# Optimization experiments

Measured on AMD Instinct MI355X. Metric: run time of the kernel, lower is better.

## Reference

```python
import jax, jax.numpy as jnp
import numpy as np

TQ, T, D = 2048, 16384, 256
H, KD, VD, DOUT = 8, 32, 32, 256


def setup_inputs() -> dict:
    key = jax.random.key(0)
    ks = jax.random.split(key, 8)
    w_scale = 1.0 / np.sqrt(D)
    return {
        "query": jax.random.normal(ks[0], (TQ, D), dtype=jnp.float32),
        "key": jax.random.normal(ks[1], (T, D), dtype=jnp.float32),
        "value": jax.random.normal(ks[2], (T, D), dtype=jnp.float32),
        "wq": jax.random.normal(ks[3], (D, H * KD), dtype=jnp.float32) * w_scale,
        "bq": jnp.zeros((H * KD,), dtype=jnp.float32),
        "wk": jax.random.normal(ks[4], (D, H * KD), dtype=jnp.float32) * w_scale,
        "bk": jnp.zeros((H * KD,), dtype=jnp.float32),
        "wv": jax.random.normal(ks[5], (D, H * VD), dtype=jnp.float32) * w_scale,
        "bv": jnp.zeros((H * VD,), dtype=jnp.float32),
        "wo": jax.random.normal(ks[6], (H * VD, DOUT), dtype=jnp.float32) * (1.0 / np.sqrt(H * VD)),
        "bo": jnp.zeros((DOUT,), dtype=jnp.float32),
    }


def reference(query, key, value, wq, bq, wk, bk, wv, bv, wo, bo):
    # Linear projections to heads: [Tq,H,KD], [T,H,KD], [T,H,VD]
    qh = (query @ wq + bq).reshape(TQ, H, KD)
    kh = (key @ wk + bk).reshape(T, H, KD)
    vh = (value @ wv + bv).reshape(T, H, VD)
    # Chunked online-softmax attention == exact softmax attention.
    # Query scaled by 1/sqrt(head_dim) as in the memory-efficient impl.
    scale = np.float32(1.0 / np.sqrt(KD))
    logits = jnp.einsum("qhd,khd->hqk", qh * scale, kh)  # [H,Tq,T]
    weights = jax.nn.softmax(logits, axis=-1)
    attn = jnp.einsum("hqk,khd->qhd", weights, vh).reshape(TQ, H * VD)
    return attn @ wo + bo  # [Tq, DOUT]
```

## Files before the change

### kernel.cpp

```cpp
#include <hip/hip_runtime.h>
#include <stdint.h>


typedef float f32x4 __attribute__((ext_vector_type(4)));
typedef __bf16 bf16x8 __attribute__((ext_vector_type(8)));

extern "C" __device__ float __ocml_native_exp2_f32(float);

__device__ __forceinline__ unsigned short f2bf(float f) {
  unsigned int u = __builtin_bit_cast(unsigned int, f);
  u += 0x7FFFu + ((u >> 16) & 1u);
  return (unsigned short)(u >> 16);
}
__device__ __forceinline__ float bf2f(unsigned u) {
  return __builtin_bit_cast(float, u << 16);
}
__device__ __forceinline__ f32x4 mfma16(bf16x8 a, bf16x8 b, f32x4 c) {
  return __builtin_amdgcn_mfma_f32_16x16x32_bf16(a, b, c, 0, 0, 0);
}
__device__ __forceinline__ float ex2(float x) {
#if __has_builtin(__builtin_amdgcn_exp2f)
  return __builtin_amdgcn_exp2f(x);
#else
  return __ocml_native_exp2_f32(x);
#endif
}
__device__ __forceinline__ unsigned pk2(float a, float b) {
  unsigned short ua = __builtin_bit_cast(unsigned short, (__bf16)a);
  unsigned short ub = __builtin_bit_cast(unsigned short, (__bf16)b);
  return (unsigned)ua | ((unsigned)ub << 16);
}
__device__ __forceinline__ uint2 pack4(f32x4 a) {
  uint2 r;
  r.x = (unsigned)f2bf(a[0]) | ((unsigned)f2bf(a[1]) << 16);
  r.y = (unsigned)f2bf(a[2]) | ((unsigned)f2bf(a[3]) << 16);
  return r;
}

#define QSCALE 0.25503483f

__global__ __launch_bounds__(256) void convert_w_kernel(
    const float* __restrict__ wq, const float* __restrict__ wk,
    const float* __restrict__ wv, const float* __restrict__ wo,
    unsigned short* __restrict__ tq, unsigned short* __restrict__ tk,
    unsigned short* __restrict__ tv, unsigned short* __restrict__ to)
{
  const int mat = blockIdx.x >> 6, k0 = (blockIdx.x & 63) * 4, n = threadIdx.x;
  const float* src; unsigned short* dst;
  if (mat == 0) { src = wq; dst = tq; }
  else if (mat == 1) { src = wk; dst = tk; }
  else if (mat == 2) { src = wv; dst = tv; }
  else { src = wo; dst = to; }
  unsigned e0 = f2bf(src[(size_t)(k0 + 0) * 256 + n]);
  unsigned e1 = f2bf(src[(size_t)(k0 + 1) * 256 + n]);
  unsigned e2 = f2bf(src[(size_t)(k0 + 2) * 256 + n]);
  unsigned e3 = f2bf(src[(size_t)(k0 + 3) * 256 + n]);
  uint2 pk = { e0 | (e1 << 16), e2 | (e3 << 16) };
  *(uint2*)&dst[(size_t)n * 256 + k0] = pk;
}

__global__ __launch_bounds__(512) void proj4_kernel(
    const float* __restrict__ Xq, const float* __restrict__ Xk,
    const float* __restrict__ Xv,
    const unsigned short* __restrict__ Wtq, const unsigned short* __restrict__ Wtk,
    const unsigned short* __restrict__ Wtv,
    const float* __restrict__ Bq, const float* __restrict__ Bk,
    const float* __restrict__ Bv,
    unsigned short* __restrict__ Oq, unsigned short* __restrict__ Ok,
    unsigned short* __restrict__ Ov)
{
  const int mat = blockIdx.y;
  const float* X; const unsigned short* Wt; const float* Bp; unsigned short* Op;
  int N; float scale; int vmode;
  if (mat == 0) {
    if (blockIdx.x >= 32) return;
    X = Xq; Wt = Wtq; Bp = Bq; Op = Oq; N = 2048; scale = QSCALE; vmode = 0;
  } else if (mat == 1) {
    X = Xk; Wt = Wtk; Bp = Bk; Op = Ok; N = 16384; scale = 1.f; vmode = 0;
  } else {
    X = Xv; Wt = Wtv; Bp = Bv; Op = Ov; N = 16384; scale = 1.f; vmode = 1;
  }
  const int tid = threadIdx.x;
  const int w = tid >> 6, lane = tid & 63, g = lane >> 4, c = lane & 15;
  const int m0 = blockIdx.x * 64;

  __shared__ __align__(16) unsigned short Xs[64 * 40];
  __shared__ __align__(16) unsigned short Ws[256 * 40];

  const f32x4 zero4 = {0.f, 0.f, 0.f, 0.f};
  f32x4 acc[4][2];
  #pragma unroll
  for (int i = 0; i < 4; ++i) { acc[i][0] = zero4; acc[i][1] = zero4; }

  const int xrow = tid >> 3, xseg = (tid & 7) * 4;
  const int wrow = tid >> 1, wseg = (tid & 1) * 16;

  for (int k0 = 0; k0 < 256; k0 += 32) {
    if (k0) __syncthreads();
    {
      float4 x = *(const float4*)&X[(size_t)(m0 + xrow) * 256 + k0 + xseg];
      uint2 px = { pk2(x.x, x.y), pk2(x.z, x.w) };
      *(uint2*)&Xs[xrow * 40 + xseg] = px;
    }
    {
      const unsigned short* wp = Wt + (size_t)wrow * 256 + k0 + wseg;
      int4 w0 = *(const int4*)wp;
      int4 w1 = *(const int4*)(wp + 8);
      *(int4*)&Ws[wrow * 40 + wseg] = w0;
      *(int4*)&Ws[wrow * 40 + wseg + 8] = w1;
    }
    __syncthreads();

    bf16x8 a[4], b[2];
    #pragma unroll
    for (int rt = 0; rt < 4; ++rt)
      a[rt] = *(const bf16x8*)&Xs[(16 * rt + c) * 40 + 8 * g];
    #pragma unroll
    for (int ct = 0; ct < 2; ++ct)
      b[ct] = *(const bf16x8*)&Ws[(32 * w + 16 * ct + c) * 40 + 8 * g];
    #pragma unroll
    for (int rt = 0; rt < 4; ++rt)
      #pragma unroll
      for (int ct = 0; ct < 2; ++ct)
        acc[rt][ct] = mfma16(a[rt], b[ct], acc[rt][ct]);
  }

  #pragma unroll
  for (int ct = 0; ct < 2; ++ct) {
    const int col = 32 * w + 16 * ct + c;
    const float bv = Bp[col];
    const int hh = col >> 5, d = col & 31;
    #pragma unroll
    for (int rt = 0; rt < 4; ++rt)
      #pragma unroll
      for (int r = 0; r < 4; ++r) {
        const int row = m0 + 16 * rt + 4 * g + r;
        const unsigned short v = f2bf((acc[rt][ct][r] + bv) * scale);
        if (vmode) {
          const int pr = (row & ~31) | (((row >> 3) & 1) << 4) |
                         (((row >> 2) & 1) << 3) | (((row >> 4) & 1) << 2) |
                         (row & 3);
          Op[((size_t)hh * 32 + d) * (size_t)N + pr] = v;
        } else {
          Op[((size_t)hh * N + row) * 32 + d] = v;
        }
      }
  }
}

__global__ __launch_bounds__(256) void attn6_kernel(
    const unsigned short* __restrict__ qh, const unsigned short* __restrict__ kh,
    const unsigned short* __restrict__ vth,
    unsigned short* __restrict__ part_o, float* __restrict__ part_l)
{
  const int f = blockIdx.x + 16 * (blockIdx.y + 8 * blockIdx.z);
  const int v = (f & 7) * 128 + (f >> 3);
  const int qb = v & 15, h = (v >> 4) & 7, sp = v >> 7;

  const int tid = threadIdx.x;
  const int w = tid >> 6, lane = tid & 63, g = lane >> 4, c = lane & 15;
  const int q0 = qb * 128 + w * 32;

  __shared__ __align__(16) unsigned short K0a[64 * 40], K0b[64 * 40];
  __shared__ __align__(16) unsigned short K1a[64 * 40], K1b[64 * 40];
  __shared__ __align__(16) unsigned short V0a[32 * 72], V0b[32 * 72];
  __shared__ __align__(16) unsigned short V1a[32 * 72], V1b[32 * 72];

  const bf16x8 qf0 = *(const bf16x8*)&qh[((size_t)h * 2048 + q0 + c) * 32 + 8 * g];
  const bf16x8 qf1 = *(const bf16x8*)&qh[((size_t)h * 2048 + q0 + 16 + c) * 32 + 8 * g];

  bf16x8 ones;
  #pragma unroll
  for (int j = 0; j < 8; ++j) ones[j] = (__bf16)1.0f;

  const f32x4 zero4 = {0.f, 0.f, 0.f, 0.f};
  f32x4 acc00 = zero4, acc01 = zero4, acc10 = zero4, acc11 = zero4;
  f32x4 accL0 = zero4, accL1 = zero4;

  const int skey = tid >> 2, sseg = (tid & 3) * 8;
  const int kwoff = skey * 40 + sseg;
  const int vrow = tid >> 3, vseg = (tid & 7) * 8;
  const int vwoff = vrow * 72 + vseg;

  const unsigned short* kp = kh + (size_t)h * 524288 +
                             ((size_t)(sp * 2048) + skey) * 32 + sseg;
  const unsigned short* vp = vth + ((size_t)h * 32 + vrow) * 16384 +
                             sp * 2048 + vseg;

  auto compute = [&](const unsigned short* Kb, const unsigned short* Vb) {
    bf16x8 kf0 = *(const bf16x8*)&Kb[(c) * 40 + 8 * g];
    bf16x8 kf1 = *(const bf16x8*)&Kb[(16 + c) * 40 + 8 * g];
    bf16x8 kf2 = *(const bf16x8*)&Kb[(32 + c) * 40 + 8 * g];
    bf16x8 kf3 = *(const bf16x8*)&Kb[(48 + c) * 40 + 8 * g];
    f32x4 s0 = mfma16(kf0, qf0, zero4);
    f32x4 s1 = mfma16(kf1, qf0, zero4);
    f32x4 s2 = mfma16(kf2, qf0, zero4);
    f32x4 s3 = mfma16(kf3, qf0, zero4);
    f32x4 t0 = mfma16(kf0, qf1, zero4);
    f32x4 t1 = mfma16(kf1, qf1, zero4);
    f32x4 t2 = mfma16(kf2, qf1, zero4);
    f32x4 t3 = mfma16(kf3, qf1, zero4);

    union { unsigned u[4]; bf16x8 v; } pa00, pa01, pa10, pa11;
    pa00.u[0] = pk2(ex2(s0[0]), ex2(s0[1]));
    pa00.u[1] = pk2(ex2(s0[2]), ex2(s0[3]));
    pa00.u[2] = pk2(ex2(s1[0]), ex2(s1[1]));
    pa00.u[3] = pk2(ex2(s1[2]), ex2(s1[3]));
    pa01.u[0] = pk2(ex2(s2[0]), ex2(s2[1]));
    pa01.u[1] = pk2(ex2(s2[2]), ex2(s2[3]));
    pa01.u[2] = pk2(ex2(s3[0]), ex2(s3[1]));
    pa01.u[3] = pk2(ex2(s3[2]), ex2(s3[3]));
    pa10.u[0] = pk2(ex2(t0[0]), ex2(t0[1]));
    pa10.u[1] = pk2(ex2(t0[2]), ex2(t0[3]));
    pa10.u[2] = pk2(ex2(t1[0]), ex2(t1[1]));
    pa10.u[3] = pk2(ex2(t1[2]), ex2(t1[3]));
    pa11.u[0] = pk2(ex2(t2[0]), ex2(t2[1]));
    pa11.u[1] = pk2(ex2(t2[2]), ex2(t2[3]));
    pa11.u[2] = pk2(ex2(t3[0]), ex2(t3[1]));
    pa11.u[3] = pk2(ex2(t3[2]), ex2(t3[3]));

    bf16x8 v00 = *(const bf16x8*)&Vb[c * 72 + 8 * g];
    bf16x8 v01 = *(const bf16x8*)&Vb[c * 72 + 32 + 8 * g];
    bf16x8 v10 = *(const bf16x8*)&Vb[(16 + c) * 72 + 8 * g];
    bf16x8 v11 = *(const bf16x8*)&Vb[(16 + c) * 72 + 32 + 8 * g];
    __builtin_amdgcn_s_setprio(1);
    acc00 = mfma16(v00, pa00.v, acc00);
    acc01 = mfma16(v10, pa00.v, acc01);
    accL0 = mfma16(ones, pa00.v, accL0);
    acc00 = mfma16(v01, pa01.v, acc00);
    acc01 = mfma16(v11, pa01.v, acc01);
    accL0 = mfma16(ones, pa01.v, accL0);
    acc10 = mfma16(v00, pa10.v, acc10);
    acc11 = mfma16(v10, pa10.v, acc11);
    accL1 = mfma16(ones, pa10.v, accL1);
    acc10 = mfma16(v01, pa11.v, acc10);
    acc11 = mfma16(v11, pa11.v, acc11);
    accL1 = mfma16(ones, pa11.v, accL1);
    __builtin_amdgcn_s_setprio(0);
  };

  {
    int4 ka = *(const int4*)kp;
    int4 va = *(const int4*)vp;
    int4 kb = *(const int4*)(kp + 2048);
    int4 vb = *(const int4*)(vp + 64);
    *(int4*)&K0a[kwoff] = ka;
    *(int4*)&V0a[vwoff] = va;
    *(int4*)&K0b[kwoff] = kb;
    *(int4*)&V0b[vwoff] = vb;
  }
  int4 kr0 = *(const int4*)(kp + 2 * 2048);
  int4 vr0 = *(const int4*)(vp + 2 * 64);
  int4 kr1 = *(const int4*)(kp + 3 * 2048);
  int4 vr1 = *(const int4*)(vp + 3 * 64);
  __syncthreads();

  for (int i = 0; i < 8; ++i) {
    *(int4*)&K1a[kwoff] = kr0;
    *(int4*)&V1a[vwoff] = vr0;
    *(int4*)&K1b[kwoff] = kr1;
    *(int4*)&V1b[vwoff] = vr1;
    {
      const int ta = (4 * i + 4) & 31, tb = (4 * i + 5) & 31;
      kr0 = *(const int4*)(kp + ta * 2048);
      vr0 = *(const int4*)(vp + ta * 64);
      kr1 = *(const int4*)(kp + tb * 2048);
      vr1 = *(const int4*)(vp + tb * 64);
    }
    compute(K0a, V0a);
    compute(K0b, V0b);
    __syncthreads();
    *(int4*)&K0a[kwoff] = kr0;
    *(int4*)&V0a[vwoff] = vr0;
    *(int4*)&K0b[kwoff] = kr1;
    *(int4*)&V0b[vwoff] = vr1;
    {
      const int ta = (4 * i + 6) & 31, tb = (4 * i + 7) & 31;
      kr0 = *(const int4*)(kp + ta * 2048);
      vr0 = *(const int4*)(vp + ta * 64);
      kr1 = *(const int4*)(kp + tb * 2048);
      vr1 = *(const int4*)(vp + tb * 64);
    }
    compute(K1a, V1a);
    compute(K1b, V1b);
    __syncthreads();
  }

  const size_t pbase = (size_t)(sp * 8 + h) * 2048;
  unsigned short* po0 = part_o + (pbase + q0 + c) * 32;
  *(uint2*)&po0[4 * g]      = pack4(acc00);
  *(uint2*)&po0[16 + 4 * g] = pack4(acc01);
  unsigned short* po1 = part_o + (pbase + q0 + 16 + c) * 32;
  *(uint2*)&po1[4 * g]      = pack4(acc10);
  *(uint2*)&po1[16 + 4 * g] = pack4(acc11);
  if (lane < 16) {
    part_l[pbase + q0 + lane]      = accL0[0];
    part_l[pbase + q0 + 16 + lane] = accL1[0];
  }
}

__global__ __launch_bounds__(512) void oproj4_kernel(
    const unsigned short* __restrict__ part_o, const float* __restrict__ part_l,
    const unsigned short* __restrict__ Wt, const float* __restrict__ bias,
    float* __restrict__ out)
{
  const int tid = threadIdx.x;
  const int w = tid >> 6, lane = tid & 63, g = lane >> 4, c = lane & 15;
  const int m0 = blockIdx.x * 64;

  __shared__ __align__(16) unsigned short As[64 * 40];
  __shared__ __align__(16) unsigned short Ws[256 * 40];

  const f32x4 zero4 = {0.f, 0.f, 0.f, 0.f};
  f32x4 acc[4][2];
  #pragma unroll
  for (int i = 0; i < 4; ++i) { acc[i][0] = zero4; acc[i][1] = zero4; }

  const int arow = tid >> 3, aseg = (tid & 7) * 4;
  const int wrow = tid >> 1, wseg = (tid & 1) * 16;

  for (int k0 = 0; k0 < 256; k0 += 32) {
    const int h = k0 >> 5;
    if (k0) __syncthreads();
    {
      float L = 0.f;
      float o0 = 0.f, o1 = 0.f, o2 = 0.f, o3 = 0.f;
      #pragma unroll
      for (int s = 0; s < 8; ++s) {
        const size_t b = (size_t)(s * 8 + h) * 2048 + m0 + arow;
        L += part_l[b];
        uint2 pk = *(const uint2*)&part_o[b * 32 + aseg];
        o0 += bf2f(pk.x & 0xffffu); o1 += bf2f(pk.x >> 16);
        o2 += bf2f(pk.y & 0xffffu); o3 += bf2f(pk.y >> 16);
      }
      const float inv = 1.f / L;
      uint2 pa = { pk2(o0 * inv, o1 * inv), pk2(o2 * inv, o3 * inv) };
      *(uint2*)&As[arow * 40 + aseg] = pa;
    }
    {
      const unsigned short* wp = Wt + (size_t)wrow * 256 + k0 + wseg;
      int4 w0 = *(const int4*)wp;
      int4 w1 = *(const int4*)(wp + 8);
      *(int4*)&Ws[wrow * 40 + wseg] = w0;
      *(int4*)&Ws[wrow * 40 + wseg + 8] = w1;
    }
    __syncthreads();

    bf16x8 a[4], b[2];
    #pragma unroll
    for (int rt = 0; rt < 4; ++rt)
      a[rt] = *(const bf16x8*)&As[(16 * rt + c) * 40 + 8 * g];
    #pragma unroll
    for (int ct = 0; ct < 2; ++ct)
      b[ct] = *(const bf16x8*)&Ws[(32 * w + 16 * ct + c) * 40 + 8 * g];
    #pragma unroll
    for (int rt = 0; rt < 4; ++rt)
      #pragma unroll
      for (int ct = 0; ct < 2; ++ct)
        acc[rt][ct] = mfma16(a[rt], b[ct], acc[rt][ct]);
  }

  #pragma unroll
  for (int ct = 0; ct < 2; ++ct) {
    const int col = 32 * w + 16 * ct + c;
    const float bv = bias[col];
    #pragma unroll
    for (int rt = 0; rt < 4; ++rt)
      #pragma unroll
      for (int r = 0; r < 4; ++r)
        out[(size_t)(m0 + 16 * rt + 4 * g + r) * 256 + col] = acc[rt][ct][r] + bv;
  }
}

extern "C" void kernel_launch(void* const* d_in, const int* in_sizes, int n_in,
                              void* d_out, int out_size, void* d_ws, size_t ws_size,
                              hipStream_t stream)
{
  (void)in_sizes; (void)n_in; (void)out_size; (void)ws_size;
  const float* query = (const float*)d_in[0];
  const float* key   = (const float*)d_in[1];
  const float* value = (const float*)d_in[2];
  const float* wq    = (const float*)d_in[3];
  const float* bq    = (const float*)d_in[4];
  const float* wk    = (const float*)d_in[5];
  const float* bk    = (const float*)d_in[6];
  const float* wv    = (const float*)d_in[7];
  const float* bv    = (const float*)d_in[8];
  const float* wo    = (const float*)d_in[9];
  const float* bo    = (const float*)d_in[10];
  float* out = (float*)d_out;

  unsigned char* ws = (unsigned char*)d_ws;
  unsigned short* qh     = (unsigned short*)(ws);
  unsigned short* khp    = (unsigned short*)(ws + 1048576);
  unsigned short* vtp    = (unsigned short*)(ws + 9437184);
  unsigned short* part_o = (unsigned short*)(ws + 17825792);
  unsigned short* wtq    = (unsigned short*)(ws + 17825792);
  unsigned short* wtk    = (unsigned short*)(ws + 17956864);
  unsigned short* wtv    = (unsigned short*)(ws + 18087936);
  float*          part_l = (float*)(ws + 26214400);
  unsigned short* wto    = (unsigned short*)(ws + 26738688);

  convert_w_kernel<<<256, 256, 0, stream>>>(wq, wk, wv, wo, wtq, wtk, wtv, wto);
  proj4_kernel<<<dim3(256, 3), 512, 0, stream>>>(
      query, key, value, wtq, wtk, wtv, bq, bk, bv, qh, khp, vtp);
  attn6_kernel<<<dim3(16, 8, 8), 256, 0, stream>>>(qh, khp, vtp, part_o, part_l);
  oproj4_kernel<<<32, 512, 0, stream>>>(part_o, part_l, wto, bo, out);
}
```

Baseline: 106.9 us.

## Shrink attention blocks, add 16-way key split, and split output projection by columns

Attention blocks drop from 256 to 128 threads and cover 64 queries each. When the workspace is large enough, the key dimension is split 16 ways instead of 8, giving many more blocks to fill the GPU. The K/V staging becomes a plain double buffer with one tile per step, and the output projection gets a second grid dimension over output columns. The float-to-bf16 packing also switches to hardware conversion. The cost is more partial outputs to write and reduce, more synchronisation steps per block, and a layout that depends on workspace size.

```diff
diff --git a/kernel.cpp b/kernel.cpp
--- a/kernel.cpp
+++ b/kernel.cpp
@@ -32,8 +32,8 @@
 }
 __device__ __forceinline__ uint2 pack4(f32x4 a) {
   uint2 r;
-  r.x = (unsigned)f2bf(a[0]) | ((unsigned)f2bf(a[1]) << 16);
-  r.y = (unsigned)f2bf(a[2]) | ((unsigned)f2bf(a[3]) << 16);
+  r.x = pk2(a[0], a[1]);
+  r.y = pk2(a[2], a[3]);
   return r;
 }
 
@@ -51,11 +51,11 @@
   else if (mat == 1) { src = wk; dst = tk; }
   else if (mat == 2) { src = wv; dst = tv; }
   else { src = wo; dst = to; }
-  unsigned e0 = f2bf(src[(size_t)(k0 + 0) * 256 + n]);
-  unsigned e1 = f2bf(src[(size_t)(k0 + 1) * 256 + n]);
-  unsigned e2 = f2bf(src[(size_t)(k0 + 2) * 256 + n]);
-  unsigned e3 = f2bf(src[(size_t)(k0 + 3) * 256 + n]);
-  uint2 pk = { e0 | (e1 << 16), e2 | (e3 << 16) };
+  float e0 = src[(size_t)(k0 + 0) * 256 + n];
+  float e1 = src[(size_t)(k0 + 1) * 256 + n];
+  float e2 = src[(size_t)(k0 + 2) * 256 + n];
+  float e3 = src[(size_t)(k0 + 3) * 256 + n];
+  uint2 pk = { pk2(e0, e1), pk2(e2, e3) };
   *(uint2*)&dst[(size_t)n * 256 + k0] = pk;
 }
 
@@ -148,23 +148,24 @@
   }
 }
 
-__global__ __launch_bounds__(256) void attn6_kernel(
+template <int NSPLIT>
+__global__ __launch_bounds__(128) void attn9_kernel(
     const unsigned short* __restrict__ qh, const unsigned short* __restrict__ kh,
     const unsigned short* __restrict__ vth,
     unsigned short* __restrict__ part_o, float* __restrict__ part_l)
 {
-  const int f = blockIdx.x + 16 * (blockIdx.y + 8 * blockIdx.z);
-  const int v = (f & 7) * 128 + (f >> 3);
-  const int qb = v & 15, h = (v >> 4) & 7, sp = v >> 7;
+  constexpr int NTILES = 256 / NSPLIT;
+  constexpr int KEYS = NTILES * 64;
+  const int f = blockIdx.x + 32 * (blockIdx.y + 8 * blockIdx.z);
+  const int v = (f & 7) * (32 * NSPLIT) + (f >> 3);
+  const int qb = v & 31, h = (v >> 5) & 7, sp = v >> 8;
 
   const int tid = threadIdx.x;
   const int w = tid >> 6, lane = tid & 63, g = lane >> 4, c = lane & 15;
-  const int q0 = qb * 128 + w * 32;
-
-  __shared__ __align__(16) unsigned short K0a[64 * 40], K0b[64 * 40];
-  __shared__ __align__(16) unsigned short K1a[64 * 40], K1b[64 * 40];
-  __shared__ __align__(16) unsigned short V0a[32 * 72], V0b[32 * 72];
-  __shared__ __align__(16) unsigned short V1a[32 * 72], V1b[32 * 72];
+  const int q0 = qb * 64 + w * 32;
+
+  __shared__ __align__(16) unsigned short Ks[2][64 * 40];
+  __shared__ __align__(16) unsigned short Vt[2][32 * 72];
 
   const bf16x8 qf0 = *(const bf16x8*)&qh[((size_t)h * 2048 + q0 + c) * 32 + 8 * g];
   const bf16x8 qf1 = *(const bf16x8*)&qh[((size_t)h * 2048 + q0 + 16 + c) * 32 + 8 * g];
@@ -177,15 +178,15 @@
   f32x4 acc00 = zero4, acc01 = zero4, acc10 = zero4, acc11 = zero4;
   f32x4 accL0 = zero4, accL1 = zero4;
 
-  const int skey = tid >> 2, sseg = (tid & 3) * 8;
-  const int kwoff = skey * 40 + sseg;
-  const int vrow = tid >> 3, vseg = (tid & 7) * 8;
+  const int krow = tid >> 1, kseg = (tid & 1) * 16;
+  const int kwoff = krow * 40 + kseg;
+  const int vrow = tid >> 2, vseg = (tid & 3) * 16;
   const int vwoff = vrow * 72 + vseg;
 
   const unsigned short* kp = kh + (size_t)h * 524288 +
-                             ((size_t)(sp * 2048) + skey) * 32 + sseg;
+                             ((size_t)(sp * KEYS) + krow) * 32 + kseg;
   const unsigned short* vp = vth + ((size_t)h * 32 + vrow) * 16384 +
-                             sp * 2048 + vseg;
+                             sp * KEYS + vseg;
 
   auto compute = [&](const unsigned short* Kb, const unsigned short* Vb) {
     bf16x8 kf0 = *(const bf16x8*)&Kb[(c) * 40 + 8 * g];
@@ -241,48 +242,34 @@
 
   {
     int4 ka = *(const int4*)kp;
+    int4 kb = *(const int4*)(kp + 8);
     int4 va = *(const int4*)vp;
-    int4 kb = *(const int4*)(kp + 2048);
-    int4 vb = *(const int4*)(vp + 64);
-    *(int4*)&K0a[kwoff] = ka;
-    *(int4*)&V0a[vwoff] = va;
-    *(int4*)&K0b[kwoff] = kb;
-    *(int4*)&V0b[vwoff] = vb;
-  }
-  int4 kr0 = *(const int4*)(kp + 2 * 2048);
-  int4 vr0 = *(const int4*)(vp + 2 * 64);
-  int4 kr1 = *(const int4*)(kp + 3 * 2048);
-  int4 vr1 = *(const int4*)(vp + 3 * 64);
+    int4 vb = *(const int4*)(vp + 8);
+    *(int4*)&Ks[0][kwoff]     = ka;
+    *(int4*)&Ks[0][kwoff + 8] = kb;
+    *(int4*)&Vt[0][vwoff]     = va;
+    *(int4*)&Vt[0][vwoff + 8] = vb;
+  }
+  int4 kr0 = *(const int4*)(kp + 2048);
+  int4 kr1 = *(const int4*)(kp + 2048 + 8);
+  int4 vr0 = *(const int4*)(vp + 64);
+  int4 vr1 = *(const int4*)(vp + 64 + 8);
   __syncthreads();
 
-  for (int i = 0; i < 8; ++i) {
-    *(int4*)&K1a[kwoff] = kr0;
-    *(int4*)&V1a[vwoff] = vr0;
-    *(int4*)&K1b[kwoff] = kr1;
-    *(int4*)&V1b[vwoff] = vr1;
-    {
-      const int ta = (4 * i + 4) & 31, tb = (4 * i + 5) & 31;
-      kr0 = *(const int4*)(kp + ta * 2048);
-      vr0 = *(const int4*)(vp + ta * 64);
-      kr1 = *(const int4*)(kp + tb * 2048);
-      vr1 = *(const int4*)(vp + tb * 64);
-    }
-    compute(K0a, V0a);
-    compute(K0b, V0b);
-    __syncthreads();
-    *(int4*)&K0a[kwoff] = kr0;
-    *(int4*)&V0a[vwoff] = vr0;
-    *(int4*)&K0b[kwoff] = kr1;
-    *(int4*)&V0b[vwoff] = vr1;
-    {
-      const int ta = (4 * i + 6) & 31, tb = (4 * i + 7) & 31;
-      kr0 = *(const int4*)(kp + ta * 2048);
-      vr0 = *(const int4*)(vp + ta * 64);
-      kr1 = *(const int4*)(kp + tb * 2048);
-      vr1 = *(const int4*)(vp + tb * 64);
-    }
-    compute(K1a, V1a);
-    compute(K1b, V1b);
+  for (int it = 0; it < NTILES; ++it) {
+    const int cur = it & 1;
+    if (it < NTILES - 1) {
+      *(int4*)&Ks[cur ^ 1][kwoff]     = kr0;
+      *(int4*)&Ks[cur ^ 1][kwoff + 8] = kr1;
+      *(int4*)&Vt[cur ^ 1][vwoff]     = vr0;
+      *(int4*)&Vt[cur ^ 1][vwoff + 8] = vr1;
+      const int t2 = (it + 2) & (NTILES - 1);
+      kr0 = *(const int4*)(kp + t2 * 2048);
+      kr1 = *(const int4*)(kp + t2 * 2048 + 8);
+      vr0 = *(const int4*)(vp + t2 * 64);
+      vr1 = *(const int4*)(vp + t2 * 64 + 8);
+    }
+    compute(&Ks[cur][0], &Vt[cur][0]);
     __syncthreads();
   }
 
@@ -299,25 +286,26 @@
   }
 }
 
-__global__ __launch_bounds__(512) void oproj4_kernel(
+template <int NSPLIT>
+__global__ __launch_bounds__(512) void oproj9_kernel(
     const unsigned short* __restrict__ part_o, const float* __restrict__ part_l,
     const unsigned short* __restrict__ Wt, const float* __restrict__ bias,
     float* __restrict__ out)
 {
   const int tid = threadIdx.x;
   const int w = tid >> 6, lane = tid & 63, g = lane >> 4, c = lane & 15;
-  const int m0 = blockIdx.x * 64;
+  const int m0 = blockIdx.x * 64, cb = blockIdx.y * 128;
 
   __shared__ __align__(16) unsigned short As[64 * 40];
-  __shared__ __align__(16) unsigned short Ws[256 * 40];
+  __shared__ __align__(16) unsigned short Ws[128 * 40];
 
   const f32x4 zero4 = {0.f, 0.f, 0.f, 0.f};
-  f32x4 acc[4][2];
-  #pragma unroll
-  for (int i = 0; i < 4; ++i) { acc[i][0] = zero4; acc[i][1] = zero4; }
+  f32x4 acc[4];
+  #pragma unroll
+  for (int i = 0; i < 4; ++i) acc[i] = zero4;
 
   const int arow = tid >> 3, aseg = (tid & 7) * 4;
-  const int wrow = tid >> 1, wseg = (tid & 1) * 16;
+  const int wrow = tid >> 2, wseg = (tid & 3) * 8;
 
   for (int k0 = 0; k0 < 256; k0 += 32) {
     const int h = k0 >> 5;
@@ -325,8 +313,8 @@
     {
       float L = 0.f;
       float o0 = 0.f, o1 = 0.f, o2 = 0.f, o3 = 0.f;
-      #pragma unroll
-      for (int s = 0; s < 8; ++s) {
+      #pragma unroll 8
+      for (int s = 0; s < NSPLIT; ++s) {
         const size_t b = (size_t)(s * 8 + h) * 2048 + m0 + arow;
         L += part_l[b];
         uint2 pk = *(const uint2*)&part_o[b * 32 + aseg];
@@ -338,45 +326,36 @@
       *(uint2*)&As[arow * 40 + aseg] = pa;
     }
     {
-      const unsigned short* wp = Wt + (size_t)wrow * 256 + k0 + wseg;
+      const unsigned short* wp = Wt + (size_t)(cb + wrow) * 256 + k0 + wseg;
       int4 w0 = *(const int4*)wp;
-      int4 w1 = *(const int4*)(wp + 8);
       *(int4*)&Ws[wrow * 40 + wseg] = w0;
-      *(int4*)&Ws[wrow * 40 + wseg + 8] = w1;
     }
     __syncthreads();
 
-    bf16x8 a[4], b[2];
+    bf16x8 a[4];
     #pragma unroll
     for (int rt = 0; rt < 4; ++rt)
       a[rt] = *(const bf16x8*)&As[(16 * rt + c) * 40 + 8 * g];
-    #pragma unroll
-    for (int ct = 0; ct < 2; ++ct)
-      b[ct] = *(const bf16x8*)&Ws[(32 * w + 16 * ct + c) * 40 + 8 * g];
-    #pragma unroll
-    for (int rt = 0; rt < 4; ++rt)
-      #pragma unroll
-      for (int ct = 0; ct < 2; ++ct)
-        acc[rt][ct] = mfma16(a[rt], b[ct], acc[rt][ct]);
-  }
-
-  #pragma unroll
-  for (int ct = 0; ct < 2; ++ct) {
-    const int col = 32 * w + 16 * ct + c;
-    const float bv = bias[col];
-    #pragma unroll
-    for (int rt = 0; rt < 4; ++rt)
-      #pragma unroll
-      for (int r = 0; r < 4; ++r)
-        out[(size_t)(m0 + 16 * rt + 4 * g + r) * 256 + col] = acc[rt][ct][r] + bv;
-  }
+    bf16x8 b = *(const bf16x8*)&Ws[(16 * w + c) * 40 + 8 * g];
+    #pragma unroll
+    for (int rt = 0; rt < 4; ++rt)
+      acc[rt] = mfma16(a[rt], b, acc[rt]);
+  }
+
+  const int col = cb + 16 * w + c;
+  const float bv = bias[col];
+  #pragma unroll
+  for (int rt = 0; rt < 4; ++rt)
+    #pragma unroll
+    for (int r = 0; r < 4; ++r)
+      out[(size_t)(m0 + 16 * rt + 4 * g + r) * 256 + col] = acc[rt][r] + bv;
 }
 
 extern "C" void kernel_launch(void* const* d_in, const int* in_sizes, int n_in,
                               void* d_out, int out_size, void* d_ws, size_t ws_size,
                               hipStream_t stream)
 {
-  (void)in_sizes; (void)n_in; (void)out_size; (void)ws_size;
+  (void)in_sizes; (void)n_in; (void)out_size;
   const float* query = (const float*)d_in[0];
   const float* key   = (const float*)d_in[1];
   const float* value = (const float*)d_in[2];
@@ -398,12 +377,19 @@
   unsigned short* wtq    = (unsigned short*)(ws + 17825792);
   unsigned short* wtk    = (unsigned short*)(ws + 17956864);
   unsigned short* wtv    = (unsigned short*)(ws + 18087936);
-  float*          part_l = (float*)(ws + 26214400);
-  unsigned short* wto    = (unsigned short*)(ws + 26738688);
+
+  const bool big = (ws_size >= 35782656ULL);
+  float*          part_l = (float*)(ws + (big ? 34603008u : 26214400u));
+  unsigned short* wto    = (unsigned short*)(ws + (big ? 35651584u : 26738688u));
 
   convert_w_kernel<<<256, 256, 0, stream>>>(wq, wk, wv, wo, wtq, wtk, wtv, wto);
   proj4_kernel<<<dim3(256, 3), 512, 0, stream>>>(
       query, key, value, wtq, wtk, wtv, bq, bk, bv, qh, khp, vtp);
-  attn6_kernel<<<dim3(16, 8, 8), 256, 0, stream>>>(qh, khp, vtp, part_o, part_l);
-  oproj4_kernel<<<32, 512, 0, stream>>>(part_o, part_l, wto, bo, out);
-}
+  if (big) {
+    attn9_kernel<16><<<dim3(32, 8, 16), 128, 0, stream>>>(qh, khp, vtp, part_o, part_l);
+    oproj9_kernel<16><<<dim3(32, 2), 512, 0, stream>>>(part_o, part_l, wto, bo, out);
+  } else {
+    attn9_kernel<8><<<dim3(32, 8, 8), 128, 0, stream>>>(qh, khp, vtp, part_o, part_l);
+    oproj9_kernel<8><<<dim3(32, 2), 512, 0, stream>>>(part_o, part_l, wto, bo, out);
+  }
+}
```

Measured after the change: 144.4 us. +35.0%, slower.
